# Performance work log

Hardware: AMD Instinct MI355X
Metric: run time of the kernel (lower is better)

## Reference

```python
import jax, jax.numpy as jnp
import numpy as np

B, S, D, H = 2, 2048, 1024, 16
DH = D // H  # 64


def setup_inputs() -> dict:
    key = jax.random.key(0)
    ks = jax.random.split(key, 10)
    inp = {
        "q": jax.random.normal(ks[0], (B, S, D), jnp.float32),
        "k": jax.random.normal(ks[1], (B, S, D), jnp.float32),
        "v": jax.random.normal(ks[2], (B, S, D), jnp.float32),
        "mask": jax.random.randint(ks[3], (B, S), 0, 2, jnp.int32),
        "Wq": jax.random.normal(ks[4], (D, D), jnp.float32) * 0.02,
        "bq": jnp.zeros((D,), jnp.float32),
        "Wk": jax.random.normal(ks[5], (D, D), jnp.float32) * 0.02,
        "bk": jnp.zeros((D,), jnp.float32),
        "Wv": jax.random.normal(ks[6], (D, D), jnp.float32) * 0.02,
        "bv": jnp.zeros((D,), jnp.float32),
    }
    return inp


def _split_heads(x):
    # [B, S, D] -> [B, H, S, DH]
    b, s, _ = x.shape
    return x.reshape(b, s, H, DH).transpose(0, 2, 1, 3)


def reference(q, k, v, mask, Wq, bq, Wk, bk, Wv, bv):
    qh = _split_heads(q @ Wq + bq)
    kh = _split_heads(k @ Wk + bk)
    vh = _split_heads(v @ Wv + bv)
    # NOTE: original scales by sqrt(hidden_size), not sqrt(head_dim)
    scores = jnp.einsum("bhqd,bhkd->bhqk", qh, kh) / jnp.sqrt(jnp.float32(D))
    m = mask.astype(jnp.float32)[:, None, None, :]  # [B,1,1,S_k]
    scores = scores + (-1e9) * (1.0 - m)
    weights = jax.nn.softmax(scores, axis=-1)
    out = jnp.einsum("bhqk,bhkd->bhqd", weights, vh)
    # concat heads: [B,H,S,DH] -> [B,S,D]
    return out.transpose(0, 2, 1, 3).reshape(q.shape[0], -1, D)
```

## Files before the change

kernel.cpp:

```cpp
#include <hip/hip_runtime.h>


#define B_ 2
#define S_ 2048
#define D_ 1024
#define H_ 16
#define DH_ 64
#define M_ (B_*S_)

#define WT_OFF  ((size_t)3*4194304)
#define XB_OFF  (WT_OFF + (size_t)3*1048576)

typedef __attribute__((ext_vector_type(8))) short short8;
typedef __attribute__((ext_vector_type(4))) float f32x4;
typedef __attribute__((ext_vector_type(4))) unsigned int u32x4;
#define MFMA16(a,b,c) __builtin_amdgcn_mfma_f32_16x16x32_bf16(a,b,c,0,0,0)

typedef __attribute__((address_space(1))) const void* gptr_t;
typedef __attribute__((address_space(3))) void* lptr_t;
static __device__ inline void gload_lds16(const void* g, void* l) {
    __builtin_amdgcn_global_load_lds((gptr_t)g, (lptr_t)l, 16, 0, 0);
}

static __device__ inline unsigned short f2bf(float x) {
    union { float f; unsigned u; } v; v.f = x;
    return (unsigned short)((v.u + 0x7fffu + ((v.u >> 16) & 1u)) >> 16);
}
static __device__ inline unsigned packp(float a, float b) {
    return __builtin_amdgcn_perm(__float_as_uint(b) + 0x8000u,
                                 __float_as_uint(a) + 0x8000u, 0x07060302u);
}

__global__ __launch_bounds__(256) void convert_all(
    const float* __restrict__ X0, const float* __restrict__ X1,
    const float* __restrict__ X2,
    const float* __restrict__ Wq, const float* __restrict__ Wk,
    const float* __restrict__ Wv,
    unsigned short* __restrict__ O0, unsigned short* __restrict__ O1,
    unsigned short* __restrict__ O2, unsigned short* __restrict__ WtBase)
{
    __shared__ unsigned short T[64][72];
    const int z = blockIdx.z;
    const int t = threadIdx.x;

    if (blockIdx.x < 4096) {
        const float* X = z==0 ? X0 : (z==1 ? X1 : X2);
        unsigned short* O = z==0 ? O0 : (z==1 ? O1 : O2);
        int idx = blockIdx.x*256 + t;
        float4 xv = *(const float4*)&X[(size_t)idx*4];
        uint2 o;
        o.x = (unsigned)f2bf(xv.x) | ((unsigned)f2bf(xv.y) << 16);
        o.y = (unsigned)f2bf(xv.z) | ((unsigned)f2bf(xv.w) << 16);
        *(uint2*)&O[(size_t)idx*4] = o;
        return;
    }

    const float* W = z==0 ? Wq : (z==1 ? Wk : Wv);
    unsigned short* Out = WtBase + ((size_t)z << 20);
    const int bx2 = blockIdx.x - 4096;
    const int n0 = (bx2 & 15)*64, k0 = (bx2 >> 4)*64;
    const int tk = t >> 4, tn4 = (t & 15)*4;

    #pragma unroll
    for (int i=0;i<4;i++){
        int kk = tk + i*16;
        float4 wv = *(const float4*)&W[(size_t)(k0+kk)*D_ + n0 + tn4];
        T[tn4+0][kk] = f2bf(wv.x);
        T[tn4+1][kk] = f2bf(wv.y);
        T[tn4+2][kk] = f2bf(wv.z);
        T[tn4+3][kk] = f2bf(wv.w);
    }
    __syncthreads();

    const int n = t >> 2, seg = t & 3;
    uint4 a = *(uint4*)&T[n][seg*16];
    uint4 b = *(uint4*)&T[n][seg*16 + 8];
    *(uint4*)&Out[(size_t)(n0+n)*D_ + k0 + seg*16]     = a;
    *(uint4*)&Out[(size_t)(n0+n)*D_ + k0 + seg*16 + 8] = b;
}

__global__ __launch_bounds__(256) void proj_gemm(
    const unsigned short* __restrict__ A0, const unsigned short* __restrict__ A1,
    const unsigned short* __restrict__ A2, const unsigned short* __restrict__ WtBase,
    const float* __restrict__ b0, const float* __restrict__ b1,
    const float* __restrict__ b2, unsigned short* __restrict__ OutBase)
{
    const int lin0 = blockIdx.x + (blockIdx.y << 3) + (blockIdx.z << 8);
    const int swz  = (lin0 & 7)*96 + (lin0 >> 3);
    const int bxn  = swz & 7;
    const int byn  = (swz >> 3) & 31;
    const int which = swz >> 8;

    const unsigned short* A  = which==0 ? A0 : (which==1 ? A1 : A2);
    const unsigned short* Bm = WtBase + ((size_t)which << 20);
    const float* bias        = which==0 ? b0 : (which==1 ? b1 : b2);
    unsigned short* Out      = OutBase + ((size_t)which << 22);
    const float oscale = (which==0) ? 0.04508422f : 1.0f;

    __shared__ __align__(16) unsigned short As[128*64];
    __shared__ __align__(16) unsigned short Bs[128*64];

    const int t    = threadIdx.x;
    const int m0   = byn * 128;
    const int n0   = bxn * 128;
    const int w    = t >> 6;
    const int lane = t & 63;
    const int l15  = lane & 15;
    const int quad = lane >> 4;
    const int wm   = w >> 1, wn = w & 1;

    f32x4 acc[4][4];
    #pragma unroll
    for (int i=0;i<4;i++)
        #pragma unroll
        for (int j=0;j<4;j++) acc[i][j] = (f32x4){0.f,0.f,0.f,0.f};

    float biasv[4];
    #pragma unroll
    for (int nt=0; nt<4; nt++)
        biasv[nt] = bias[n0 + wn*64 + nt*16 + l15];

    int sArow[4], sAkc[4];
    #pragma unroll
    for (int i=0;i<4;i++){
        int s  = (w*4 + i)*64 + lane;
        int r  = s >> 3, cs = s & 7;
        sArow[i] = r;
        sAkc[i]  = ((cs ^ (r & 7)) * 8);
    }

    for (int ks = 0; ks < 16; ++ks) {
        const int kb = ks * 64;
        #pragma unroll
        for (int i=0;i<4;i++){
            int s = (w*4 + i)*64 + lane;
            gload_lds16(A  + (size_t)(m0 + sArow[i])*D_ + kb + sAkc[i], (unsigned short*)As + s*8);
            gload_lds16(Bm + (size_t)(n0 + sArow[i])*D_ + kb + sAkc[i], (unsigned short*)Bs + s*8);
        }
        __syncthreads();

        #pragma unroll
        for (int kh=0; kh<2; kh++){
            short8 aF[4], bF[4];
            #pragma unroll
            for (int mt=0; mt<4; mt++){
                int r  = wm*64 + mt*16 + l15;
                int cs = (kh*4 + quad) ^ (r & 7);
                aF[mt] = *(const short8*)(As + r*64 + cs*8);
            }
            #pragma unroll
            for (int nt=0; nt<4; nt++){
                int r  = wn*64 + nt*16 + l15;
                int cs = (kh*4 + quad) ^ (r & 7);
                bF[nt] = *(const short8*)(Bs + r*64 + cs*8);
            }
            #pragma unroll
            for (int mt=0; mt<4; mt++)
                #pragma unroll
                for (int nt=0; nt<4; nt++)
                    acc[mt][nt] = MFMA16(aF[mt], bF[nt], acc[mt][nt]);
        }
        __syncthreads();
    }

    if (which != 2) {
        #pragma unroll
        for (int nt=0; nt<4; nt++){
            int n  = n0 + wn*64 + nt*16 + l15;
            int hh = n >> 6, dh = n & 63;
            #pragma unroll
            for (int mt=0; mt<4; mt++){
                #pragma unroll
                for (int r=0; r<4; r++){
                    int m  = m0 + wm*64 + mt*16 + quad*4 + r;
                    int bb = m >> 11, ss = m & (S_-1);
                    float v = (acc[mt][nt][r] + biasv[nt]) * oscale;
                    Out[((size_t)((bb*H_ + hh)*S_ + ss))*DH_ + dh] = f2bf(v);
                }
            }
        }
    } else {
        #pragma unroll
        for (int nt=0; nt<4; nt++){
            int n  = n0 + wn*64 + nt*16 + l15;
            int hh = n >> 6, dh = n & 63;
            #pragma unroll
            for (int mt=0; mt<4; mt++){
                int m  = m0 + wm*64 + mt*16 + quad*4;
                int bb = m >> 11, ss = m & (S_-1);
                uint2 pk;
                pk.x = packp(acc[mt][nt][0] + biasv[nt], acc[mt][nt][1] + biasv[nt]);
                pk.y = packp(acc[mt][nt][2] + biasv[nt], acc[mt][nt][3] + biasv[nt]);
                *(uint2*)&Out[((size_t)((bb*H_ + hh)*DH_ + dh))*S_ + ss] = pk;
            }
        }
    }
}

__global__ __launch_bounds__(512, 2) void attn_kernel(
    const unsigned short* __restrict__ ws, const int* __restrict__ mask,
    float* __restrict__ out)
{
    const unsigned short* Qh = ws;
    const unsigned short* Kh = ws + (size_t)M_*D_;
    const unsigned short* Vg = ws + 2*(size_t)M_*D_;

    const int lin = blockIdx.x + (blockIdx.y << 3) + (blockIdx.z << 7);
    const int Wn  = (lin & 7)*32 + (lin >> 3);
    const int qt = Wn & 7;
    const int h  = (Wn >> 3) & 15;
    const int bb = Wn >> 7;

    const size_t base = ((size_t)(bb*H_ + h)) * S_ * DH_;
    const int q0 = qt * 256;

    __shared__ __align__(16) unsigned char smem[73728];
    unsigned short* KsB = (unsigned short*)smem;
    unsigned short* VtB = (unsigned short*)(smem + 32768);
    float*          MsT = (float*)(smem + 65536);
    float*          Ob  = (float*)smem;

    const int t    = threadIdx.x;
    const int w    = t >> 6;
    const int lane = t & 63;
    const int l15  = lane & 15;
    const int quad = lane >> 4;

    short8 qf[2][2];
    #pragma unroll
    for (int qs=0; qs<2; qs++){
        const unsigned short* qp = Qh + base + (size_t)(q0 + w*32 + qs*16 + l15)*DH_ + quad*8;
        qf[qs][0] = *(const short8*)(qp);
        qf[qs][1] = *(const short8*)(qp + 32);
    }

    f32x4 accO[2][4];
    #pragma unroll
    for (int qs=0; qs<2; qs++)
        #pragma unroll
        for (int i=0;i<4;i++) accO[qs][i] = (f32x4){0.f,0.f,0.f,0.f};
    f32x4 lv[2] = {(f32x4){0.f,0.f,0.f,0.f}, (f32x4){0.f,0.f,0.f,0.f}};

    int rr[2], cc[2], ssl[2], gK[2];
    #pragma unroll
    for (int i=0;i<2;i++){
        int s  = (w*2 + i)*64 + lane;
        int r  = s >> 3, cs = s & 7;
        int r6 = r & 63;
        ssl[i] = s;
        rr[i]  = r;
        cc[i]  = (cs ^ (r & 7)) * 8;
        gK[i]  = (r & 64) + ((r6 >> 4) & 1)*32 + ((r6 >> 2) & 3)*8 + (r6 >> 5)*4 + (r6 & 3);
    }

    #define ISSUE128(k0v, p) do {                                              \
        _Pragma("unroll")                                                      \
        for (int i=0;i<2;i++){                                                 \
            gload_lds16(Kh + base + (size_t)((k0v) + gK[i])*DH_ + cc[i],       \
                        KsB + (p)*8192 + ssl[i]*8);                            \
            gload_lds16(Vg + base + (size_t)(rr[i] & 63)*S_ + (k0v)            \
                            + (rr[i] & 64) + cc[i],                            \
                        VtB + (p)*8192 + ssl[i]*8);                            \
        }                                                                      \
    } while(0)

    ISSUE128(0, 0);
    #pragma unroll
    for (int i=0;i<4;i++){
        int idx = i*512 + t;
        MsT[idx] = mask[bb*S_ + idx] ? 0.f : -1e9f;
    }
    __syncthreads();

    for (int it = 0; it < 16; ++it){
        const int p = it & 1;
        if (it < 15) ISSUE128((it+1)*128, 1-p);

        #pragma unroll
        for (int sb = 0; sb < 2; ++sb){
            const unsigned short* Ks  = KsB + p*8192 + sb*4096;
            const unsigned short* Vts = VtB + p*8192 + sb*4096;
            const float*          Mp  = MsT + it*128 + sb*64;

            f32x4 msv[4];
            #pragma unroll
            for (int st=0; st<4; st++)
                msv[st] = *(const f32x4*)&Mp[(st&1)*32 + (st>>1)*4 + quad*8];

            short8 ka[4], kb[4];
            #pragma unroll
            for (int st=0; st<4; st++){
                int row = st*16 + l15;
                const unsigned short* kr = Ks + row*64;
                ka[st] = *(const short8*)(kr + ((quad    ) ^ (row & 7))*8);
                kb[st] = *(const short8*)(kr + ((quad + 4) ^ (row & 7))*8);
            }
            short8 vf[4][2];
            #pragma unroll
            for (int mt=0; mt<4; mt++){
                int row = mt*16 + l15;
                const unsigned short* vr = Vts + row*64;
                vf[mt][0] = *(const short8*)(vr + ((quad    ) ^ (row & 7))*8);
                vf[mt][1] = *(const short8*)(vr + ((quad + 4) ^ (row & 7))*8);
            }

            #pragma unroll
            for (int qs=0; qs<2; qs++){
                f32x4 sc[4];
                __builtin_amdgcn_s_setprio(1);
                #pragma unroll
                for (int st=0; st<4; st++){
                    f32x4 a = msv[st];
                    a = MFMA16(ka[st], qf[qs][0], a);
                    a = MFMA16(kb[st], qf[qs][1], a);
                    sc[st] = a;
                }
                __builtin_amdgcn_s_setprio(0);
                f32x4 pvv[4];
                #pragma unroll
                for (int st=0; st<4; st++)
                    #pragma unroll
                    for (int rj=0; rj<4; rj++)
                        pvv[st][rj] = __builtin_amdgcn_exp2f(sc[st][rj]);
                f32x4 s01 = pvv[0] + pvv[1];
                f32x4 s23 = pvv[2] + pvv[3];
                lv[qs] += (s01 + s23);
                u32x4 u0 = { packp(pvv[0][0],pvv[0][1]), packp(pvv[0][2],pvv[0][3]),
                             packp(pvv[2][0],pvv[2][1]), packp(pvv[2][2],pvv[2][3]) };
                u32x4 u1 = { packp(pvv[1][0],pvv[1][1]), packp(pvv[1][2],pvv[1][3]),
                             packp(pvv[3][0],pvv[3][1]), packp(pvv[3][2],pvv[3][3]) };
                short8 pf0 = __builtin_bit_cast(short8, u0);
                short8 pf1 = __builtin_bit_cast(short8, u1);
                __builtin_amdgcn_s_setprio(1);
                #pragma unroll
                for (int mt=0; mt<4; mt++){
                    accO[qs][mt] = MFMA16(vf[mt][0], pf0, accO[qs][mt]);
                    accO[qs][mt] = MFMA16(vf[mt][1], pf1, accO[qs][mt]);
                }
                __builtin_amdgcn_s_setprio(0);
            }
        }
        __syncthreads();
    }

    #pragma unroll
    for (int qs=0; qs<2; qs++){
        float l = (lv[qs][0] + lv[qs][1]) + (lv[qs][2] + lv[qs][3]);
        l += __shfl_xor(l, 16);
        l += __shfl_xor(l, 32);
        float invl = 1.0f / fmaxf(l, 1e-30f);
        #pragma unroll
        for (int mt=0; mt<4; mt++)
            #pragma unroll
            for (int r=0; r<4; r++)
                Ob[(w*32 + qs*16 + l15)*68 + mt*16 + quad*4 + r] = accO[qs][mt][r]*invl;
    }
    __syncthreads();

    #pragma unroll
    for (int i=0;i<8;i++){
        int f  = (i*512 + t)*4;
        int qq = f >> 6, dh = f & 63;
        float4 o = *(float4*)&Ob[qq*68 + dh];
        *(float4*)&out[((size_t)(bb*S_ + q0 + qq))*D_ + h*DH_ + dh] = o;
    }
    #undef ISSUE128
}

extern "C" void kernel_launch(void* const* d_in, const int* in_sizes, int n_in,
                              void* d_out, int out_size, void* d_ws, size_t ws_size,
                              hipStream_t stream) {
    const float* q    = (const float*)d_in[0];
    const float* k    = (const float*)d_in[1];
    const float* v    = (const float*)d_in[2];
    const int*   mask = (const int*)d_in[3];
    const float* Wq   = (const float*)d_in[4];
    const float* b0   = (const float*)d_in[5];
    const float* Wk   = (const float*)d_in[6];
    const float* b1   = (const float*)d_in[7];
    const float* Wv   = (const float*)d_in[8];
    const float* b2   = (const float*)d_in[9];
    float* out = (float*)d_out;
    unsigned short* ws = (unsigned short*)d_ws;

    unsigned short* xq = ws + XB_OFF;
    unsigned short* xk = (unsigned short*)d_out;
    unsigned short* xv = (unsigned short*)d_out + 4194304;

    convert_all<<<dim3(4352,1,3), 256, 0, stream>>>(q, k, v, Wq, Wk, Wv,
                                                    xq, xk, xv, ws + WT_OFF);
    proj_gemm<<<dim3(8,32,3), 256, 0, stream>>>(xq, xk, xv, ws + WT_OFF,
                                                b0, b1, b2, ws);
    attn_kernel<<<dim3(8,16,2), 512, 0, stream>>>(ws, mask, out);
}
```

Measured before the change: 198.5 us.

## Split key tile across wave pairs, each wave covering 64 query rows

Reorganizes attention work so each pair of waves shares 64 query rows and splits every 128-key tile in half, instead of each wave handling 32 rows over the full tile. Each wave now reads only half the K/V fragments from LDS per iteration while reusing them across four query sub-tiles, which cuts LDS read traffic per MFMA. Partial outputs and row sums from the two waves are combined through shared memory at the end, with normalization moved into the store loop. The larger register footprint required dropping launch bounds occupancy from 2 to 1 blocks per CU.

```diff
diff --git a/kernel.cpp b/kernel.cpp
--- a/kernel.cpp
+++ b/kernel.cpp
@@ -197,7 +197,7 @@
     }
 }
 
-__global__ __launch_bounds__(512, 2) void attn_kernel(
+__global__ __launch_bounds__(512, 1) void attn_kernel(
     const unsigned short* __restrict__ ws, const int* __restrict__ mask,
     float* __restrict__ out)
 {
@@ -219,27 +219,33 @@
     unsigned short* VtB = (unsigned short*)(smem + 32768);
     float*          MsT = (float*)(smem + 65536);
     float*          Ob  = (float*)smem;
+    float*          Lb  = (float*)(smem + 69632);
+    float*          invL= (float*)(smem + 71680);
 
     const int t    = threadIdx.x;
     const int w    = t >> 6;
     const int lane = t & 63;
     const int l15  = lane & 15;
     const int quad = lane >> 4;
-
-    short8 qf[2][2];
-    #pragma unroll
-    for (int qs=0; qs<2; qs++){
-        const unsigned short* qp = Qh + base + (size_t)(q0 + w*32 + qs*16 + l15)*DH_ + quad*8;
+    const int qw   = w >> 1;
+    const int pb   = w & 1;
+
+    short8 qf[4][2];
+    #pragma unroll
+    for (int qs=0; qs<4; qs++){
+        const unsigned short* qp = Qh + base + (size_t)(q0 + qw*64 + qs*16 + l15)*DH_ + quad*8;
         qf[qs][0] = *(const short8*)(qp);
         qf[qs][1] = *(const short8*)(qp + 32);
     }
 
-    f32x4 accO[2][4];
-    #pragma unroll
-    for (int qs=0; qs<2; qs++)
+    f32x4 accO[4][4];
+    #pragma unroll
+    for (int qs=0; qs<4; qs++)
         #pragma unroll
         for (int i=0;i<4;i++) accO[qs][i] = (f32x4){0.f,0.f,0.f,0.f};
-    f32x4 lv[2] = {(f32x4){0.f,0.f,0.f,0.f}, (f32x4){0.f,0.f,0.f,0.f}};
+    f32x4 lv[4];
+    #pragma unroll
+    for (int qs=0; qs<4; qs++) lv[qs] = (f32x4){0.f,0.f,0.f,0.f};
 
     int rr[2], cc[2], ssl[2], gK[2];
     #pragma unroll
@@ -276,85 +282,103 @@
         const int p = it & 1;
         if (it < 15) ISSUE128((it+1)*128, 1-p);
 
-        #pragma unroll
-        for (int sb = 0; sb < 2; ++sb){
-            const unsigned short* Ks  = KsB + p*8192 + sb*4096;
-            const unsigned short* Vts = VtB + p*8192 + sb*4096;
-            const float*          Mp  = MsT + it*128 + sb*64;
-
-            f32x4 msv[4];
+        const unsigned short* Ks  = KsB + p*8192 + pb*4096;
+        const unsigned short* Vts = VtB + p*8192 + pb*4096;
+        const float*          Mp  = MsT + it*128 + pb*64;
+
+        f32x4 msv[4];
+        #pragma unroll
+        for (int st=0; st<4; st++)
+            msv[st] = *(const f32x4*)&Mp[(st&1)*32 + (st>>1)*4 + quad*8];
+
+        short8 ka[4], kb[4];
+        #pragma unroll
+        for (int st=0; st<4; st++){
+            int row = st*16 + l15;
+            const unsigned short* kr = Ks + row*64;
+            ka[st] = *(const short8*)(kr + ((quad    ) ^ (row & 7))*8);
+            kb[st] = *(const short8*)(kr + ((quad + 4) ^ (row & 7))*8);
+        }
+        short8 vf[4][2];
+        #pragma unroll
+        for (int mt=0; mt<4; mt++){
+            int row = mt*16 + l15;
+            const unsigned short* vr = Vts + row*64;
+            vf[mt][0] = *(const short8*)(vr + ((quad    ) ^ (row & 7))*8);
+            vf[mt][1] = *(const short8*)(vr + ((quad + 4) ^ (row & 7))*8);
+        }
+
+        #pragma unroll
+        for (int qs=0; qs<4; qs++){
+            f32x4 sc[4];
+            __builtin_amdgcn_s_setprio(1);
+            #pragma unroll
+            for (int st=0; st<4; st++){
+                f32x4 a = msv[st];
+                a = MFMA16(ka[st], qf[qs][0], a);
+                a = MFMA16(kb[st], qf[qs][1], a);
+                sc[st] = a;
+            }
+            __builtin_amdgcn_s_setprio(0);
+            f32x4 pvv[4];
             #pragma unroll
             for (int st=0; st<4; st++)
-                msv[st] = *(const f32x4*)&Mp[(st&1)*32 + (st>>1)*4 + quad*8];
-
-            short8 ka[4], kb[4];
-            #pragma unroll
-            for (int st=0; st<4; st++){
-                int row = st*16 + l15;
-                const unsigned short* kr = Ks + row*64;
-                ka[st] = *(const short8*)(kr + ((quad    ) ^ (row & 7))*8);
-                kb[st] = *(const short8*)(kr + ((quad + 4) ^ (row & 7))*8);
-            }
-            short8 vf[4][2];
+                #pragma unroll
+                for (int rj=0; rj<4; rj++)
+                    pvv[st][rj] = __builtin_amdgcn_exp2f(sc[st][rj]);
+            f32x4 s01 = pvv[0] + pvv[1];
+            f32x4 s23 = pvv[2] + pvv[3];
+            lv[qs] += (s01 + s23);
+            u32x4 u0 = { packp(pvv[0][0],pvv[0][1]), packp(pvv[0][2],pvv[0][3]),
+                         packp(pvv[2][0],pvv[2][1]), packp(pvv[2][2],pvv[2][3]) };
+            u32x4 u1 = { packp(pvv[1][0],pvv[1][1]), packp(pvv[1][2],pvv[1][3]),
+                         packp(pvv[3][0],pvv[3][1]), packp(pvv[3][2],pvv[3][3]) };
+            short8 pf0 = __builtin_bit_cast(short8, u0);
+            short8 pf1 = __builtin_bit_cast(short8, u1);
+            __builtin_amdgcn_s_setprio(1);
             #pragma unroll
             for (int mt=0; mt<4; mt++){
-                int row = mt*16 + l15;
-                const unsigned short* vr = Vts + row*64;
-                vf[mt][0] = *(const short8*)(vr + ((quad    ) ^ (row & 7))*8);
-                vf[mt][1] = *(const short8*)(vr + ((quad + 4) ^ (row & 7))*8);
-            }
-
-            #pragma unroll
-            for (int qs=0; qs<2; qs++){
-                f32x4 sc[4];
-                __builtin_amdgcn_s_setprio(1);
-                #pragma unroll
-                for (int st=0; st<4; st++){
-                    f32x4 a = msv[st];
-                    a = MFMA16(ka[st], qf[qs][0], a);
-                    a = MFMA16(kb[st], qf[qs][1], a);
-                    sc[st] = a;
-                }
-                __builtin_amdgcn_s_setprio(0);
-                f32x4 pvv[4];
-                #pragma unroll
-                for (int st=0; st<4; st++)
-                    #pragma unroll
-                    for (int rj=0; rj<4; rj++)
-                        pvv[st][rj] = __builtin_amdgcn_exp2f(sc[st][rj]);
-                f32x4 s01 = pvv[0] + pvv[1];
-                f32x4 s23 = pvv[2] + pvv[3];
-                lv[qs] += (s01 + s23);
-                u32x4 u0 = { packp(pvv[0][0],pvv[0][1]), packp(pvv[0][2],pvv[0][3]),
-                             packp(pvv[2][0],pvv[2][1]), packp(pvv[2][2],pvv[2][3]) };
-                u32x4 u1 = { packp(pvv[1][0],pvv[1][1]), packp(pvv[1][2],pvv[1][3]),
-                             packp(pvv[3][0],pvv[3][1]), packp(pvv[3][2],pvv[3][3]) };
-                short8 pf0 = __builtin_bit_cast(short8, u0);
-                short8 pf1 = __builtin_bit_cast(short8, u1);
-                __builtin_amdgcn_s_setprio(1);
-                #pragma unroll
-                for (int mt=0; mt<4; mt++){
-                    accO[qs][mt] = MFMA16(vf[mt][0], pf0, accO[qs][mt]);
-                    accO[qs][mt] = MFMA16(vf[mt][1], pf1, accO[qs][mt]);
-                }
-                __builtin_amdgcn_s_setprio(0);
-            }
+                accO[qs][mt] = MFMA16(vf[mt][0], pf0, accO[qs][mt]);
+                accO[qs][mt] = MFMA16(vf[mt][1], pf1, accO[qs][mt]);
+            }
+            __builtin_amdgcn_s_setprio(0);
         }
         __syncthreads();
     }
 
-    #pragma unroll
-    for (int qs=0; qs<2; qs++){
+    float lpart[4];
+    #pragma unroll
+    for (int qs=0; qs<4; qs++){
         float l = (lv[qs][0] + lv[qs][1]) + (lv[qs][2] + lv[qs][3]);
         l += __shfl_xor(l, 16);
         l += __shfl_xor(l, 32);
-        float invl = 1.0f / fmaxf(l, 1e-30f);
-        #pragma unroll
-        for (int mt=0; mt<4; mt++)
-            #pragma unroll
-            for (int r=0; r<4; r++)
-                Ob[(w*32 + qs*16 + l15)*68 + mt*16 + quad*4 + r] = accO[qs][mt][r]*invl;
-    }
+        lpart[qs] = l;
+    }
+    if (quad == 0){
+        #pragma unroll
+        for (int qs=0; qs<4; qs++)
+            Lb[pb*256 + qw*64 + qs*16 + l15] = lpart[qs];
+    }
+    if (pb == 0){
+        #pragma unroll
+        for (int qs=0; qs<4; qs++)
+            #pragma unroll
+            for (int mt=0; mt<4; mt++)
+                #pragma unroll
+                for (int r=0; r<4; r++)
+                    Ob[(qw*64 + qs*16 + l15)*68 + mt*16 + quad*4 + r] = accO[qs][mt][r];
+    }
+    __syncthreads();
+    if (pb == 1){
+        #pragma unroll
+        for (int qs=0; qs<4; qs++)
+            #pragma unroll
+            for (int mt=0; mt<4; mt++)
+                #pragma unroll
+                for (int r=0; r<4; r++)
+                    Ob[(qw*64 + qs*16 + l15)*68 + mt*16 + quad*4 + r] += accO[qs][mt][r];
+    }
+    if (t < 256) invL[t] = 1.0f / fmaxf(Lb[t] + Lb[256 + t], 1e-30f);
     __syncthreads();
 
     #pragma unroll
@@ -362,6 +386,8 @@
         int f  = (i*512 + t)*4;
         int qq = f >> 6, dh = f & 63;
         float4 o = *(float4*)&Ob[qq*68 + dh];
+        float s = invL[qq];
+        o.x *= s; o.y *= s; o.z *= s; o.w *= s;
         *(float4*)&out[((size_t)(bb*S_ + q0 + qq))*D_ + h*DH_ + dh] = o;
     }
     #undef ISSUE128
```

Result: no change. 201.5 us (+1.5%).
